# Kernel optimization log

Measured on AMD Instinct MI355X. Metric: run time of the kernel, lower is better.

## Reference

```python
import jax, jax.numpy as jnp
import numpy as np

S, DIM, H, HD = 8192, 1280, 16, 80
B, L = 8, 1024  # 8 equal-length packed segments


def setup_inputs() -> dict:
    key = jax.random.key(0)
    ks = jax.random.split(key, 6)
    hidden_states = jax.random.normal(ks[0], (S, DIM), dtype=jnp.float32)
    Wqkv = jax.random.normal(ks[1], (DIM, 3 * DIM), dtype=jnp.float32) * (DIM ** -0.5)
    bqkv = jax.random.normal(ks[2], (3 * DIM,), dtype=jnp.float32) * 0.02
    Wproj = jax.random.normal(ks[3], (DIM, DIM), dtype=jnp.float32) * (DIM ** -0.5)
    bproj = jax.random.normal(ks[4], (DIM,), dtype=jnp.float32) * 0.02
    # rotary tables: per-token position within its segment, repeated-half layout
    pos = jnp.tile(jnp.arange(L, dtype=jnp.float32), B)  # [S]
    inv_freq = 1.0 / (10000.0 ** (jnp.arange(0, HD, 2, dtype=jnp.float32) / HD))  # [HD/2]
    ang = pos[:, None] * inv_freq[None, :]  # [S, HD/2]
    ang = jnp.concatenate([ang, ang], axis=-1)  # [S, HD]
    cos, sin = jnp.cos(ang), jnp.sin(ang)
    cu_seqlens = (jnp.arange(B + 1, dtype=jnp.int32) * L)
    return {"hidden_states": hidden_states, "cos": cos, "sin": sin,
            "Wqkv": Wqkv, "bqkv": bqkv, "Wproj": Wproj, "bproj": bproj,
            "cu_seqlens": cu_seqlens, "max_seqlen": L}


def _rotate_half(x):
    x1, x2 = jnp.split(x, 2, axis=-1)
    return jnp.concatenate([-x2, x1], axis=-1)


def reference(hidden_states, cos, sin, Wqkv, bqkv, Wproj, bproj, cu_seqlens, max_seqlen):
    s = hidden_states.shape[0]
    nseg = cu_seqlens.shape[0] - 1
    scale = HD ** -0.5
    qkv = (hidden_states @ Wqkv + bqkv).reshape(s, 3, H, HD)
    q, k, v = qkv[:, 0], qkv[:, 1], qkv[:, 2]  # each [S, H, HD]
    c = cos[:, None, :]
    sn = sin[:, None, :]
    q = q * c + _rotate_half(q) * sn
    k = k * c + _rotate_half(k) * sn
    # equal-length packed segments: [S,H,HD] -> [B,L,H,HD]
    q = q.reshape(nseg, max_seqlen, H, HD)
    k = k.reshape(nseg, max_seqlen, H, HD)
    v = v.reshape(nseg, max_seqlen, H, HD)
    scores = jnp.einsum("blhd,bmhd->bhlm", q, k) * scale
    probs = jax.nn.softmax(scores, axis=-1)
    out = jnp.einsum("bhlm,bmhd->blhd", probs, v).reshape(s, DIM)
    return out @ Wproj + bproj
```

## Files before the change

### kernel.cpp

```cpp
#include <hip/hip_runtime.h>
#include <hip/hip_bf16.h>
#include <stdint.h>

typedef __bf16 bf16_t;
typedef __bf16 bf16x8 __attribute__((ext_vector_type(8)));
typedef float f32x4 __attribute__((ext_vector_type(4)));
typedef float f32x16 __attribute__((ext_vector_type(16)));

#define S_TOK 8192
#define DIM   1280
#define NH    16
#define HD    80
#define LSEQ  1024
#define N_QKV 3840

__device__ __forceinline__ int qk_perm(int n) {
  if (n >= 2560) return n;
  int base = (n / 80) * 80, j = n - base;
  return base + ((j & 1) ? (j >> 1) + 40 : (j >> 1));
}

__device__ __forceinline__ void gload16(const bf16_t* g, void* l) {
  __builtin_amdgcn_global_load_lds(
      (__attribute__((address_space(1))) uint32_t*)g,
      (__attribute__((address_space(3))) uint32_t*)l, 16, 0, 0);
}

__global__ __launch_bounds__(256) void k_conv_bf16(const float* __restrict__ in,
                                                   bf16_t* __restrict__ out) {
  int g = blockIdx.x * 256 + threadIdx.x;
  const float4* p = reinterpret_cast<const float4*>(in) + (size_t)g * 2;
  float4 v0 = p[0], v1 = p[1];
  bf16x8 o;
  o[0] = (bf16_t)v0.x; o[1] = (bf16_t)v0.y; o[2] = (bf16_t)v0.z; o[3] = (bf16_t)v0.w;
  o[4] = (bf16_t)v1.x; o[5] = (bf16_t)v1.y; o[6] = (bf16_t)v1.z; o[7] = (bf16_t)v1.w;
  *reinterpret_cast<bf16x8*>(out + (size_t)g * 8) = o;
}

__global__ __launch_bounds__(256) void k_transpose_bf16(const float* __restrict__ W,
                                                        bf16_t* __restrict__ Wt,
                                                        int K, int N) {
  __shared__ float tile[32][33];
  int n0 = blockIdx.x * 32, k0 = blockIdx.y * 32;
  int tx = threadIdx.x, ty = threadIdx.y;
#pragma unroll
  for (int j = 0; j < 32; j += 8)
    tile[ty + j][tx] = W[(size_t)(k0 + ty + j) * N + n0 + tx];
  __syncthreads();
#pragma unroll
  for (int j = 0; j < 32; j += 8)
    Wt[(size_t)(n0 + ty + j) * K + k0 + tx] = (bf16_t)tile[tx][ty + j];
}

template <bool OUT_BF16, bool ROPE>
__global__ __launch_bounds__(512, 2) void k_gemm8(const bf16_t* __restrict__ A,
                                                  const bf16_t* __restrict__ Bt,
                                                  const float* __restrict__ bias,
                                                  void* __restrict__ Cout,
                                                  int N,
                                                  const float* __restrict__ cosT,
                                                  const float* __restrict__ sinT) {
  constexpr int K = 1280;
  constexpr int NT = K / 64;
  const float QS = 0.11180339887498949f * 1.4426950408889634f;
  __shared__ __align__(16) char smem[131072];
  const int nb = N >> 8;
  const int cpx = (int)gridDim.x >> 3;
  const int wg = ((int)blockIdx.x & 7) * cpx + ((int)blockIdx.x >> 3);
  const int bm = wg / nb, bn = wg % nb;
  const int tid = threadIdx.x, lane = tid & 63, w = tid >> 6;
  const int wm = w >> 2, wn = w & 3;
  const int l15 = lane & 15, lg = lane >> 4;

  const bf16_t* Ab = A + (size_t)(bm * 256) * K;

  const int srow = w * 8 + (lane >> 3);
  const int scol = ((lane & 7) ^ (lane >> 3)) * 8;

  int srowB[4];
#pragma unroll
  for (int g = 0; g < 4; ++g) {
    int n = bn * 256 + g * 64 + srow;
    srowB[g] = ROPE ? qk_perm(n) : n;
  }

  float bv4[4];
#pragma unroll
  for (int nf = 0; nf < 4; ++nf) {
    int col = bn * 256 + wn * 64 + nf * 16 + l15;
    bv4[nf] = bias[ROPE ? qk_perm(col) : col];
  }
  asm volatile("" :: "v"(bv4[0]), "v"(bv4[1]), "v"(bv4[2]), "v"(bv4[3]) : "memory");

  char* const sm = smem;
  auto stageA = [&](int buf, int g, int k0) {
    gload16(Ab + (size_t)(g * 64 + srow) * K + k0 + scol,
            sm + buf * 65536 + g * 8192 + w * 1024);
  };
  auto stageB = [&](int buf, int g, int k0) {
    gload16(Bt + (size_t)srowB[g] * K + k0 + scol,
            sm + buf * 65536 + 32768 + g * 8192 + w * 1024);
  };

  f32x4 acc[8][4];
#pragma unroll
  for (int i = 0; i < 8; ++i)
#pragma unroll
    for (int j = 0; j < 4; ++j) acc[i][j] = (f32x4){0.f, 0.f, 0.f, 0.f};

#pragma unroll
  for (int g = 0; g < 4; ++g) { stageA(0, g, 0); stageB(0, g, 0); }
  asm volatile("s_waitcnt vmcnt(0)\n\ts_barrier" ::: "memory");

#pragma unroll 1
  for (int T = 0; T < NT; ++T) {
    const int buf = T & 1, nbuf = buf ^ 1;
    const int k1 = (T + 1) * 64;
    if (T + 1 < NT) {
#pragma unroll
      for (int g = 0; g < 4; ++g) { stageA(nbuf, g, k1); stageB(nbuf, g, k1); }
    }
    const char* Abase = sm + buf * 65536;
    const char* Bbase = Abase + 32768;
#pragma unroll
    for (int kk = 0; kk < 2; ++kk) {
      const int cb = kk * 64 + lg * 16;
      bf16x8 bfv[4];
#pragma unroll
      for (int nf = 0; nf < 4; ++nf) {
        const int row = wn * 64 + nf * 16 + l15;
        bfv[nf] = *reinterpret_cast<const bf16x8*>(Bbase + row * 128 + (cb ^ ((row & 7) << 4)));
      }
#pragma unroll
      for (int mg = 0; mg < 2; ++mg) {
        bf16x8 af[4];
#pragma unroll
        for (int mf = 0; mf < 4; ++mf) {
          const int row = wm * 128 + mg * 64 + mf * 16 + l15;
          af[mf] = *reinterpret_cast<const bf16x8*>(Abase + row * 128 + (cb ^ ((row & 7) << 4)));
        }
        __builtin_amdgcn_s_setprio(1);
#pragma unroll
        for (int mf = 0; mf < 4; ++mf)
#pragma unroll
          for (int nf = 0; nf < 4; ++nf)
            acc[mg * 4 + mf][nf] =
                __builtin_amdgcn_mfma_f32_16x16x32_bf16(af[mf], bfv[nf], acc[mg * 4 + mf][nf], 0, 0, 0);
        __builtin_amdgcn_s_setprio(0);
      }
    }
    if (T + 1 < NT) {
      asm volatile("s_waitcnt vmcnt(0)\n\ts_barrier" ::: "memory");
    }
  }

  float* ldsC = reinterpret_cast<float*>(sm);
  float* ldsS = reinterpret_cast<float*>(sm + 45056);
  if (ROPE) {
    __syncthreads();
#pragma unroll
    for (int i = 0; i < 5; ++i) {
      int c = tid + i * 512;
      int row = c / 10, q4 = c - row * 10;
      float4 vc = *reinterpret_cast<const float4*>(cosT + (size_t)(bm * 256 + row) * 80 + q4 * 4);
      float4 vs = *reinterpret_cast<const float4*>(sinT + (size_t)(bm * 256 + row) * 80 + q4 * 4);
      *reinterpret_cast<float4*>(ldsC + row * 44 + q4 * 4) = vc;
      *reinterpret_cast<float4*>(ldsS + row * 44 + q4 * 4) = vs;
    }
    __syncthreads();
  }

  const int rg = lg << 2;
#pragma unroll
  for (int nf = 0; nf < 4; ++nf) {
    const int col = bn * 256 + wn * 64 + nf * 16 + l15;
    const float bv = bv4[nf];
    const bool isqk = ROPE && (col < 2560);
    const bool isq  = col < 1280;
    const int pi = (col % 80) >> 1;
    const float sgn = (l15 & 1) ? 1.f : -1.f;
#pragma unroll
    for (int m8 = 0; m8 < 8; ++m8) {
      const int row0 = bm * 256 + wm * 128 + m8 * 16 + rg;
      const int lrow0 = wm * 128 + m8 * 16 + rg;
#pragma unroll
      for (int r = 0; r < 4; ++r) {
        float v = acc[m8][nf][r] + bv;
        if (isqk) {
          float other = __shfl_xor(v, 1);
          float c = ldsC[(lrow0 + r) * 44 + pi];
          float s = ldsS[(lrow0 + r) * 44 + pi];
          v = v * c + sgn * other * s;
          if (isq) v *= QS;
        }
        const int orow = row0 + r;
        if (OUT_BF16)
          reinterpret_cast<bf16_t*>(Cout)[(size_t)orow * N + col] = (bf16_t)v;
        else
          reinterpret_cast<float*>(Cout)[(size_t)orow * N + col] = v;
      }
    }
  }
}

__global__ __launch_bounds__(256) void k_vtrans(const bf16_t* __restrict__ qkv,
                                                bf16_t* __restrict__ vtg) {
  __shared__ bf16_t T[64][88];
  int sh = blockIdx.x >> 4;
  int kt = blockIdx.x & 15;
  int seg = sh >> 4, h = sh & 15;
  int kv0 = kt * 64;
  int tid = threadIdx.x;
#pragma unroll
  for (int i = 0; i < 3; ++i) {
    int c = tid + i * 256;
    if (c < 640) {
      int r = c / 10, ch = c - r * 10;
      *reinterpret_cast<uint4*>(&T[r][ch * 8]) =
        *reinterpret_cast<const uint4*>(qkv + (size_t)(seg * 1024 + kv0 + r) * N_QKV + 2 * DIM + h * 80 + ch * 8);
    }
  }
  __syncthreads();
#pragma unroll
  for (int i = 0; i < 3; ++i) {
    int c = tid + i * 256;
    if (c < 640) {
      int d = c >> 3, co = c & 7;
      bf16x8 o;
#pragma unroll
      for (int j = 0; j < 8; ++j) {
        int kp = co * 8 + j;
        int kv = (kp & ~12) | (((kp >> 2) & 1) << 3) | (((kp >> 3) & 1) << 2);
        o[j] = T[kv][d];
      }
      *reinterpret_cast<bf16x8*>(vtg + ((size_t)(sh * 80 + d)) * 1024 + kv0 + co * 8) = o;
    }
  }
}

__global__ __launch_bounds__(512, 2) void k_attn2(const bf16_t* __restrict__ qkv,
                                                  const bf16_t* __restrict__ vtg,
                                                  bf16_t* __restrict__ outp) {
  __shared__ __align__(16) char smem[69632];
  bf16_t* KsB = (bf16_t*)smem;
  bf16_t* VsB = (bf16_t*)(smem + 32768);

  const int bid = blockIdx.x;
  const int seg = bid & 7, qt = (bid >> 3) & 3, h = bid >> 5;
  const int tid = threadIdx.x, lane = tid & 63, w = tid >> 6;
  const int l31 = lane & 31, hi = lane >> 5;
  const int sw = l31 & 7;
  const int q0 = seg * 1024 + qt * 256;

  const bf16_t* kbase = qkv + ((size_t)seg * 1024) * N_QKV + DIM + h * 80;
  const bf16_t* vbase = vtg + ((size_t)(seg * 16 + h) * 80) * 1024;

  bf16x8 qf[5];
  {
    const bf16_t* qp = qkv + (size_t)(q0 + w * 32 + l31) * N_QKV + h * 80 + hi * 8;
#pragma unroll
    for (int ks = 0; ks < 5; ++ks) qf[ks] = *reinterpret_cast<const bf16x8*>(qp + ks * 16);
  }

  const uint4 ones4 = {0x3F803F80u, 0x3F803F80u, 0x3F803F80u, 0x3F803F80u};
  uint4 kreg[2], vreg[2];
  auto issue = [&](int kv0) {
#pragma unroll
    for (int i = 0; i < 2; ++i) {
      int c = tid + i * 512;
      if (c < 640) {
        int r = c / 10, ch = c - r * 10;
        kreg[i] = *reinterpret_cast<const uint4*>(kbase + (size_t)(kv0 + r) * N_QKV + ch * 8);
      }
    }
#pragma unroll
    for (int i = 0; i < 2; ++i) {
      int c = tid + i * 512;
      if (c < 768) {
        int d = c >> 3, ch = c & 7;
        uint4 v = {0u, 0u, 0u, 0u};
        if (d < 80) v = *reinterpret_cast<const uint4*>(vbase + (size_t)d * 1024 + kv0 + ch * 8);
        else if (d == 80) v = ones4;
        vreg[i] = v;
      }
    }
  };
  auto commit = [&](int kb, int vb) {
    bf16_t* Kb = KsB + kb * 8192;
    bf16_t* Vb = VsB + vb * 6144;
#pragma unroll
    for (int i = 0; i < 2; ++i) {
      int c = tid + i * 512;
      if (c < 640) {
        int r = c / 10, ch = c - r * 10;
        *reinterpret_cast<uint4*>(Kb + r * 128 + ((ch ^ (r & 7)) << 3)) = kreg[i];
      }
    }
#pragma unroll
    for (int i = 0; i < 2; ++i) {
      int c = tid + i * 512;
      if (c < 768) {
        int d = c >> 3, ch = c & 7;
        *reinterpret_cast<uint4*>(Vb + d * 64 + ((ch ^ (d & 7)) << 3)) = vreg[i];
      }
    }
  };

  f32x16 o0, o1, o2;
#pragma unroll
  for (int r = 0; r < 16; ++r) { o0[r] = 0.f; o1[r] = 0.f; o2[r] = 0.f; }
  float mrun = -1e30f;
  f32x16 st0, st1;
  bf16x8 pb[4];

  auto qk = [&](int kb) {
#pragma unroll
    for (int r = 0; r < 16; ++r) { st0[r] = 0.f; st1[r] = 0.f; }
    const bf16_t* Kb = KsB + kb * 8192;
    __builtin_amdgcn_s_setprio(1);
#pragma unroll
    for (int ks = 0; ks < 5; ++ks) {
      const int so = (((ks << 1) | hi) ^ sw) << 3;
      bf16x8 k0 = *reinterpret_cast<const bf16x8*>(Kb + l31 * 128 + so);
      bf16x8 k1 = *reinterpret_cast<const bf16x8*>(Kb + (32 + l31) * 128 + so);
      st0 = __builtin_amdgcn_mfma_f32_32x32x16_bf16(k0, qf[ks], st0, 0, 0, 0);
      st1 = __builtin_amdgcn_mfma_f32_32x32x16_bf16(k1, qf[ks], st1, 0, 0, 0);
    }
    __builtin_amdgcn_s_setprio(0);
  };
  auto pv = [&](int vb) {
    const bf16_t* Vb = VsB + vb * 6144;
    __builtin_amdgcn_s_setprio(1);
#pragma unroll
    for (int ks2 = 0; ks2 < 4; ++ks2) {
      const int so = (((ks2 << 1) | hi) ^ sw) << 3;
      bf16x8 v0 = *reinterpret_cast<const bf16x8*>(Vb + l31 * 64 + so);
      bf16x8 v1 = *reinterpret_cast<const bf16x8*>(Vb + (32 + l31) * 64 + so);
      bf16x8 v2 = *reinterpret_cast<const bf16x8*>(Vb + (64 + l31) * 64 + so);
      o0 = __builtin_amdgcn_mfma_f32_32x32x16_bf16(v0, pb[ks2], o0, 0, 0, 0);
      o1 = __builtin_amdgcn_mfma_f32_32x32x16_bf16(v1, pb[ks2], o1, 0, 0, 0);
      o2 = __builtin_amdgcn_mfma_f32_32x32x16_bf16(v2, pb[ks2], o2, 0, 0, 0);
    }
    __builtin_amdgcn_s_setprio(0);
  };
  auto softmax_pack = [&]() {
    float mt[16];
#pragma unroll
    for (int r = 0; r < 16; ++r) mt[r] = fmaxf(st0[r], st1[r]);
#pragma unroll
    for (int s2 = 8; s2 >= 1; s2 >>= 1)
#pragma unroll
      for (int r = 0; r < s2; ++r) mt[r] = fmaxf(mt[r], mt[r + s2]);
    float mx = fmaxf(mt[0], __shfl_xor(mt[0], 32));
    if (!__all(mx <= mrun + 6.0f)) {
      float mnew = fmaxf(mrun, mx);
      float corr = __builtin_exp2f(mrun - mnew);
      mrun = mnew;
#pragma unroll
      for (int r = 0; r < 16; ++r) { o0[r] *= corr; o1[r] *= corr; o2[r] *= corr; }
    }
#pragma unroll
    for (int r = 0; r < 16; ++r) st0[r] = __builtin_exp2f(st0[r] - mrun);
#pragma unroll
    for (int r = 0; r < 16; ++r) st1[r] = __builtin_exp2f(st1[r] - mrun);
#pragma unroll
    for (int u = 0; u < 2; ++u)
#pragma unroll
      for (int j = 0; j < 8; ++j) {
        pb[u][j]     = (bf16_t)st0[u * 8 + j];
        pb[2 + u][j] = (bf16_t)st1[u * 8 + j];
      }
  };

  issue(0);
  commit(0, 0);
  __syncthreads();
  issue(64);
  qk(0);
  softmax_pack();
  commit(1, 1);
  __syncthreads();

#pragma unroll 1
  for (int t = 1; t < 16; ++t) {
    if (t < 15) issue((t + 1) * 64);
    qk(t & 1);
    pv((t - 1) % 3);
    softmax_pack();
    if (t < 15) commit((t + 1) & 1, (t + 1) % 3);
    __syncthreads();
  }
  pv(0);
  __syncthreads();

  float sp = o2[8] + __shfl_xor(o2[8], 32);
  float inv = 1.0f / sp;

  bf16_t* Osm = (bf16_t*)smem;
  const int qrow = w * 32 + l31;
#pragma unroll
  for (int r = 0; r < 16; ++r) {
    int crow = (r & 3) + 8 * (r >> 2) + 4 * hi;
    Osm[qrow * 88 + crow]      = (bf16_t)(o0[r] * inv);
    Osm[qrow * 88 + 32 + crow] = (bf16_t)(o1[r] * inv);
    if (r < 8) Osm[qrow * 88 + 64 + crow] = (bf16_t)(o2[r] * inv);
  }
  __syncthreads();
#pragma unroll
  for (int i = 0; i < 5; ++i) {
    int c = tid + i * 512;
    int q = c / 10, ch = c - q * 10;
    uint4 v = *reinterpret_cast<const uint4*>(Osm + q * 88 + ch * 8);
    *reinterpret_cast<uint4*>(outp + (size_t)(q0 + q) * DIM + h * 80 + ch * 8) = v;
  }
}

extern "C" void kernel_launch(void* const* d_in, const int* in_sizes, int n_in,
                              void* d_out, int out_size, void* d_ws, size_t ws_size,
                              hipStream_t stream) {
  const float* hs    = (const float*)d_in[0];
  const float* cosT  = (const float*)d_in[1];
  const float* sinT  = (const float*)d_in[2];
  const float* Wqkv  = (const float*)d_in[3];
  const float* bqkv  = (const float*)d_in[4];
  const float* Wproj = (const float*)d_in[5];
  const float* bproj = (const float*)d_in[6];
  (void)in_sizes; (void)n_in; (void)out_size; (void)ws_size;

  char* ws = (char*)d_ws;
  bf16_t* hsb  = (bf16_t*)(ws);
  bf16_t* w1t  = (bf16_t*)(ws + 20971520);
  bf16_t* w2t  = (bf16_t*)(ws + 30801920);
  bf16_t* qkvb = (bf16_t*)(ws + 34078720);
  bf16_t* attn = (bf16_t*)(ws + 96993280);
  bf16_t* vtg  = hsb;

  k_conv_bf16<<<5120, 256, 0, stream>>>(hs, hsb);
  k_transpose_bf16<<<dim3(120, 40), dim3(32, 8), 0, stream>>>(Wqkv, w1t, 1280, 3840);
  k_transpose_bf16<<<dim3(40, 40), dim3(32, 8), 0, stream>>>(Wproj, w2t, 1280, 1280);
  k_gemm8<true, true><<<480, 512, 0, stream>>>(hsb, w1t, bqkv, (void*)qkvb, 3840, cosT, sinT);
  k_vtrans<<<2048, 256, 0, stream>>>(qkvb, vtg);
  k_attn2<<<512, 512, 0, stream>>>(qkvb, vtg, attn);
  k_gemm8<false, false><<<160, 512, 0, stream>>>(attn, w2t, bproj, d_out, 1280, nullptr, nullptr);
}
```

Measured before the change: 250.7 us.

## Stage attention K/V tiles with direct global-to-LDS async loads

The attention kernel stops staging K and V tiles through registers followed by LDS writes. It now uses global_load_lds to copy 16-byte chunks straight into swizzled LDS buffers, precomputing per-lane source and destination addresses. The ones/zero padding rows for V are read from a small buffer filled by a new init kernel, which reuses the Wqkv transpose workspace. The GEMM epilogue is also split with if constexpr so the non-RoPE path drops the dead RoPE branch. This frees registers and issue slots, but the copies now depend on vmcnt and barrier ordering for correctness.

```diff
diff --git a/kernel.cpp b/kernel.cpp
--- a/kernel.cpp
+++ b/kernel.cpp
@@ -154,9 +154,11 @@
     }
   }
 
-  float* ldsC = reinterpret_cast<float*>(sm);
-  float* ldsS = reinterpret_cast<float*>(sm + 45056);
-  if (ROPE) {
+  const int rg = lg << 2;
+
+  if constexpr (ROPE) {
+    float* ldsC = reinterpret_cast<float*>(sm);
+    float* ldsS = reinterpret_cast<float*>(sm + 45056);
     __syncthreads();
 #pragma unroll
     for (int i = 0; i < 5; ++i) {
@@ -168,36 +170,49 @@
       *reinterpret_cast<float4*>(ldsS + row * 44 + q4 * 4) = vs;
     }
     __syncthreads();
-  }
-
-  const int rg = lg << 2;
-#pragma unroll
-  for (int nf = 0; nf < 4; ++nf) {
-    const int col = bn * 256 + wn * 64 + nf * 16 + l15;
-    const float bv = bv4[nf];
-    const bool isqk = ROPE && (col < 2560);
-    const bool isq  = col < 1280;
-    const int pi = (col % 80) >> 1;
-    const float sgn = (l15 & 1) ? 1.f : -1.f;
-#pragma unroll
-    for (int m8 = 0; m8 < 8; ++m8) {
-      const int row0 = bm * 256 + wm * 128 + m8 * 16 + rg;
-      const int lrow0 = wm * 128 + m8 * 16 + rg;
-#pragma unroll
-      for (int r = 0; r < 4; ++r) {
-        float v = acc[m8][nf][r] + bv;
-        if (isqk) {
-          float other = __shfl_xor(v, 1);
-          float c = ldsC[(lrow0 + r) * 44 + pi];
-          float s = ldsS[(lrow0 + r) * 44 + pi];
-          v = v * c + sgn * other * s;
-          if (isq) v *= QS;
+
+#pragma unroll
+    for (int nf = 0; nf < 4; ++nf) {
+      const int col = bn * 256 + wn * 64 + nf * 16 + l15;
+      const float bv = bv4[nf];
+      const bool isqk = col < 2560;
+      const bool isq  = col < 1280;
+      const int pi = (col % 80) >> 1;
+      const float sgn = (l15 & 1) ? 1.f : -1.f;
+#pragma unroll
+      for (int m8 = 0; m8 < 8; ++m8) {
+        const int row0 = bm * 256 + wm * 128 + m8 * 16 + rg;
+        const int lrow0 = wm * 128 + m8 * 16 + rg;
+#pragma unroll
+        for (int r = 0; r < 4; ++r) {
+          float v = acc[m8][nf][r] + bv;
+          if (isqk) {
+            float other = __shfl_xor(v, 1);
+            float c = ldsC[(lrow0 + r) * 44 + pi];
+            float s = ldsS[(lrow0 + r) * 44 + pi];
+            v = v * c + sgn * other * s;
+            if (isq) v *= QS;
+          }
+          reinterpret_cast<bf16_t*>(Cout)[(size_t)(row0 + r) * N + col] = (bf16_t)v;
         }
-        const int orow = row0 + r;
-        if (OUT_BF16)
-          reinterpret_cast<bf16_t*>(Cout)[(size_t)orow * N + col] = (bf16_t)v;
-        else
-          reinterpret_cast<float*>(Cout)[(size_t)orow * N + col] = v;
+      }
+    }
+  } else {
+#pragma unroll
+    for (int nf = 0; nf < 4; ++nf) {
+      const int col = bn * 256 + wn * 64 + nf * 16 + l15;
+      const float bv = bv4[nf];
+#pragma unroll
+      for (int m8 = 0; m8 < 8; ++m8) {
+        const int row0 = bm * 256 + wm * 128 + m8 * 16 + rg;
+#pragma unroll
+        for (int r = 0; r < 4; ++r) {
+          float v = acc[m8][nf][r] + bv;
+          if (OUT_BF16)
+            reinterpret_cast<bf16_t*>(Cout)[(size_t)(row0 + r) * N + col] = (bf16_t)v;
+          else
+            reinterpret_cast<float*>(Cout)[(size_t)(row0 + r) * N + col] = v;
+        }
       }
     }
   }
@@ -238,12 +253,18 @@
   }
 }
 
+__global__ __launch_bounds__(256) void k_padinit(bf16_t* __restrict__ vpad) {
+  int g = blockIdx.x * 256 + threadIdx.x;
+  const uint4 ones4 = {0x3F803F80u, 0x3F803F80u, 0x3F803F80u, 0x3F803F80u};
+  const uint4 z4 = {0u, 0u, 0u, 0u};
+  reinterpret_cast<uint4*>(vpad)[g] = (g < 128) ? ones4 : z4;
+}
+
 __global__ __launch_bounds__(512, 2) void k_attn2(const bf16_t* __restrict__ qkv,
                                                   const bf16_t* __restrict__ vtg,
+                                                  const bf16_t* __restrict__ vpad,
                                                   bf16_t* __restrict__ outp) {
   __shared__ __align__(16) char smem[69632];
-  bf16_t* KsB = (bf16_t*)smem;
-  bf16_t* VsB = (bf16_t*)(smem + 32768);
 
   const int bid = blockIdx.x;
   const int seg = bid & 7, qt = (bid >> 3) & 3, h = bid >> 5;
@@ -262,48 +283,32 @@
     for (int ks = 0; ks < 5; ++ks) qf[ks] = *reinterpret_cast<const bf16x8*>(qp + ks * 16);
   }
 
-  const uint4 ones4 = {0x3F803F80u, 0x3F803F80u, 0x3F803F80u, 0x3F803F80u};
-  uint4 kreg[2], vreg[2];
-  auto issue = [&](int kv0) {
-#pragma unroll
-    for (int i = 0; i < 2; ++i) {
-      int c = tid + i * 512;
-      if (c < 640) {
-        int r = c / 10, ch = c - r * 10;
-        kreg[i] = *reinterpret_cast<const uint4*>(kbase + (size_t)(kv0 + r) * N_QKV + ch * 8);
-      }
-    }
-#pragma unroll
-    for (int i = 0; i < 2; ++i) {
-      int c = tid + i * 512;
-      if (c < 768) {
-        int d = c >> 3, ch = c & 7;
-        uint4 v = {0u, 0u, 0u, 0u};
-        if (d < 80) v = *reinterpret_cast<const uint4*>(vbase + (size_t)d * 1024 + kv0 + ch * 8);
-        else if (d == 80) v = ones4;
-        vreg[i] = v;
-      }
-    }
-  };
-  auto commit = [&](int kb, int vb) {
-    bf16_t* Kb = KsB + kb * 8192;
-    bf16_t* Vb = VsB + vb * 6144;
-#pragma unroll
-    for (int i = 0; i < 2; ++i) {
-      int c = tid + i * 512;
-      if (c < 640) {
-        int r = c / 10, ch = c - r * 10;
-        *reinterpret_cast<uint4*>(Kb + r * 128 + ((ch ^ (r & 7)) << 3)) = kreg[i];
-      }
-    }
-#pragma unroll
-    for (int i = 0; i < 2; ++i) {
-      int c = tid + i * 512;
-      if (c < 768) {
-        int d = c >> 3, ch = c & 7;
-        *reinterpret_cast<uint4*>(Vb + d * 64 + ((ch ^ (d & 7)) << 3)) = vreg[i];
-      }
-    }
+  const int kr0 = 8 * w + (lane >> 4);
+  const int kr1 = kr0 + 4;
+  const bf16_t* kSrc0 = kbase + (size_t)kr0 * N_QKV + (((lane & 15) ^ (kr0 & 7)) << 3);
+  const bf16_t* kSrc1 = kbase + (size_t)kr1 * N_QKV + (((lane & 15) ^ (kr1 & 7)) << 3);
+  const int kDst0 = 2 * w * 1024, kDst1 = kDst0 + 1024;
+  const int vcofs = (((lane & 7) ^ (lane >> 3)) << 3);
+  const int vd0 = 8 * w + (lane >> 3);
+  const bf16_t* vSrc0 = vbase + (size_t)vd0 * 1024 + vcofs;
+  const int vDst0 = w * 1024;
+  const bf16_t* vSrc1 = nullptr;
+  int vDst1 = 0;
+  if (w < 4) {
+    const int d1 = 64 + 8 * w + (lane >> 3);
+    vSrc1 = (d1 < 80) ? (vbase + (size_t)d1 * 1024 + vcofs)
+                      : (vpad + (size_t)(d1 - 80) * 1024 + vcofs);
+    vDst1 = (8 + w) * 1024;
+  }
+
+  auto gstage = [&](int kv0, int kb, int vb) {
+    char* Kb = smem + kb * 16384;
+    char* Vb = smem + 32768 + vb * 12288;
+    const size_t kadv = (size_t)kv0 * N_QKV;
+    gload16(kSrc0 + kadv, Kb + kDst0);
+    gload16(kSrc1 + kadv, Kb + kDst1);
+    gload16(vSrc0 + kv0, Vb + vDst0);
+    if (w < 4) gload16(vSrc1 + kv0, Vb + vDst1);
   };
 
   f32x16 o0, o1, o2;
@@ -316,7 +321,7 @@
   auto qk = [&](int kb) {
 #pragma unroll
     for (int r = 0; r < 16; ++r) { st0[r] = 0.f; st1[r] = 0.f; }
-    const bf16_t* Kb = KsB + kb * 8192;
+    const bf16_t* Kb = (const bf16_t*)(smem + kb * 16384);
     __builtin_amdgcn_s_setprio(1);
 #pragma unroll
     for (int ks = 0; ks < 5; ++ks) {
@@ -329,7 +334,7 @@
     __builtin_amdgcn_s_setprio(0);
   };
   auto pv = [&](int vb) {
-    const bf16_t* Vb = VsB + vb * 6144;
+    const bf16_t* Vb = (const bf16_t*)(smem + 32768 + vb * 12288);
     __builtin_amdgcn_s_setprio(1);
 #pragma unroll
     for (int ks2 = 0; ks2 < 4; ++ks2) {
@@ -372,22 +377,19 @@
       }
   };
 
-  issue(0);
-  commit(0, 0);
-  __syncthreads();
-  issue(64);
+  gstage(0, 0, 0);
+  __syncthreads();
+  gstage(64, 1, 1);
   qk(0);
   softmax_pack();
-  commit(1, 1);
   __syncthreads();
 
 #pragma unroll 1
   for (int t = 1; t < 16; ++t) {
-    if (t < 15) issue((t + 1) * 64);
+    if (t < 15) gstage((t + 1) * 64, (t + 1) & 1, (t + 1) % 3);
     qk(t & 1);
     pv((t - 1) % 3);
     softmax_pack();
-    if (t < 15) commit((t + 1) & 1, (t + 1) % 3);
     __syncthreads();
   }
   pv(0);
@@ -434,12 +436,14 @@
   bf16_t* qkvb = (bf16_t*)(ws + 34078720);
   bf16_t* attn = (bf16_t*)(ws + 96993280);
   bf16_t* vtg  = hsb;
+  bf16_t* vpad = w1t;
 
   k_conv_bf16<<<5120, 256, 0, stream>>>(hs, hsb);
   k_transpose_bf16<<<dim3(120, 40), dim3(32, 8), 0, stream>>>(Wqkv, w1t, 1280, 3840);
   k_transpose_bf16<<<dim3(40, 40), dim3(32, 8), 0, stream>>>(Wproj, w2t, 1280, 1280);
   k_gemm8<true, true><<<480, 512, 0, stream>>>(hsb, w1t, bqkv, (void*)qkvb, 3840, cosT, sinT);
+  k_padinit<<<8, 256, 0, stream>>>(vpad);
   k_vtrans<<<2048, 256, 0, stream>>>(qkvb, vtg);
-  k_attn2<<<512, 512, 0, stream>>>(qkvb, vtg, attn);
+  k_attn2<<<512, 512, 0, stream>>>(qkvb, vtg, vpad, attn);
   k_gemm8<false, false><<<160, 512, 0, stream>>>(attn, w2t, bproj, d_out, 1280, nullptr, nullptr);
 }
```

Measured after the change: 233.3 us. -6.9%, faster.
